# Kernel tuning notes

Measured on AMD Instinct MI355X. Metric: run time of the kernel, lower is better.

Reference implementation:

```python
import jax, jax.numpy as jnp
import numpy as np

G, N, DEG = 64, 2048, 8          # graphs, nodes/graph, avg degree
NTOT = G * N                      # 131072 nodes
E = NTOT * DEG                    # 1048576 edges
K = int(np.ceil(0.2 * N))         # 410 nodes kept per graph (SAGPooling ratio=0.2)
NK = G * K                        # 26240 pooled nodes
H, C = 3, 20                      # GAT heads, per-head channels
NEG_BIG = jnp.float32(-1e30)


def gcn(x, src, dst, W, b, n):
    """PyG GCNConv: x' = D^-1/2 (A+I) D^-1/2 x W + b (edge weight 1)."""
    h = x @ W
    deg = jax.ops.segment_sum(jnp.ones(src.shape[0], x.dtype), dst, num_segments=n) + 1.0
    dinv = jax.lax.rsqrt(deg)
    coef = dinv[src] * dinv[dst]                    # [E]
    agg = jax.ops.segment_sum(h[src] * coef[:, None], dst, num_segments=n)
    agg = agg + h * (dinv * dinv)[:, None]          # self loops
    return agg + b


def setup_inputs() -> dict:
    key = jax.random.key(0)
    ks = jax.random.split(key, 16)
    # edges constrained within each graph: per-graph local indices + offsets
    off = jnp.repeat(jnp.arange(G, dtype=jnp.int32) * N, N * DEG)   # [E]
    src = jax.random.randint(ks[0], (E,), 0, N, dtype=jnp.int32) + off
    dst = jax.random.randint(ks[1], (E,), 0, N, dtype=jnp.int32) + off
    batch = jnp.repeat(jnp.arange(G, dtype=jnp.int32), N)           # [NTOT]
    x = jax.random.normal(ks[2], (NTOT, 5), jnp.float32)
    s = 0.1
    return {
        "x": x, "src": src, "dst": dst, "batch": batch,
        "W1": jax.random.normal(ks[3], (5, 10)) * s,   "b1": jnp.zeros((10,)),
        "Ws": jax.random.normal(ks[4], (10, 1)) * s,   "bs": jnp.zeros((1,)),
        "Wg": jax.random.normal(ks[5], (10, H * C)) * s,
        "a_src": jax.random.normal(ks[6], (H, C)) * s,
        "a_dst": jax.random.normal(ks[7], (H, C)) * s,
        "bg": jnp.zeros((H * C,)),
        "Wf1": jax.random.normal(ks[8], (60, 30)) * s, "bf1": jnp.zeros((30,)),
        "Wf2": jax.random.normal(ks[9], (30, 3)) * s,  "bf2": jnp.zeros((3,)),
    }


def reference(x, src, dst, batch, W1, b1, Ws, bs, Wg, a_src, a_dst, bg, Wf1, bf1, Wf2, bf2):
    n = x.shape[0]
    # GCNConv(5,10)
    x1 = gcn(x, src, dst, W1, b1, n)                              # [NTOT,10]
    # SAGPooling: GCN scorer, top-k per graph, gate by tanh(score)
    score = gcn(x1, src, dst, Ws, bs, n)[:, 0]                    # [NTOT]
    _, topi = jax.lax.top_k(score.reshape(G, N), K)               # [G,K]
    perm = (topi + (jnp.arange(G) * N)[:, None]).reshape(-1)      # [NK] global ids
    xp = x1[perm] * jnp.tanh(score[perm])[:, None]                # [NK,10]
    # remap edges; drop (mask) edges touching removed nodes (filter_adj)
    new_idx = jnp.full((n,), -1, jnp.int32).at[perm].set(jnp.arange(NK, dtype=jnp.int32))
    s2, d2 = new_idx[src], new_idx[dst]
    emask = (s2 >= 0) & (d2 >= 0)
    s2 = jnp.where(emask, s2, 0)
    d2 = jnp.where(emask, d2, 0)
    # GATConv(10, 20, heads=3) with self loops
    h = (xp @ Wg).reshape(NK, H, C)
    al_s = jnp.sum(h * a_src, -1)                                 # [NK,H]
    al_d = jnp.sum(h * a_dst, -1)
    loop = jnp.arange(NK, dtype=jnp.int32)
    sa = jnp.concatenate([s2, loop])
    da = jnp.concatenate([d2, loop])
    ma = jnp.concatenate([emask, jnp.ones((NK,), bool)])
    logits = jax.nn.leaky_relu(al_s[sa] + al_d[da], 0.2)          # [E+NK,H]
    logits = jnp.where(ma[:, None], logits, NEG_BIG)
    mx = jax.ops.segment_max(logits, da, num_segments=NK)         # finite: self loops
    w = jnp.exp(logits - mx[da]) * ma[:, None]
    denom = jax.ops.segment_sum(w, da, num_segments=NK)
    alpha = w / denom[da]                                         # edge softmax
    out = jax.ops.segment_sum(h[sa] * alpha[..., None], da, num_segments=NK)  # [NK,H,C]
    xg = out.reshape(NK, H * C) + bg                              # concat heads -> 60
    # scatter_add readout over graphs
    g = jax.ops.segment_sum(xg, batch[perm], num_segments=G)      # [G,60]
    # MLP + LogSoftmax
    z = jax.nn.relu(g @ Wf1 + bf1) @ Wf2 + bf2                    # [G,3]
    return jax.nn.log_softmax(z, axis=1)
```

## Files before the change

kernel.cpp:

```cpp
#include <hip/hip_runtime.h>
#include <math.h>

#define G    64
#define NPG  2048
#define NTOT (G * NPG)
#define EPG  (NPG * 8)
#define NE   (NTOT * 8)
#define KSEL 410
#define NH   3
#define NC   20
#define HC   60
#define FCAP 24
#define KPAD 512
#define RP   12

#define OFF_H1P   0
#define OFF_CSR   98304
#define OFF_HIST  131072
#define OFF_RS    139264
#define OFF_SK    147456
#define OFF_NEWL  155648
#define OFF_PERML 159744
#define OFF_WSUM  160568
#define OFF_FLAGS 160632
#define OFF_BUFK  160656
#define OFF_BUFI  160912
#define ARENA_SZ  161040
#define OFF_XP    0
#define OFF_FADJ  16400
#define OFF_FCNT  36080
#define OFF_HF    37728
#define OFF_ALS   139264
#define OFF_ALD   144184
#define OFF_WRED  149104
#define OFF_GOUT  151024
#define OFF_HID   151264

__device__ inline float leaky(float x) { return x >= 0.f ? x : 0.2f * x; }

__device__ inline int wave_incl_scan(int v) {
    int lane = threadIdx.x & 63;
#pragma unroll
    for (int d = 1; d < 64; d <<= 1) {
        int t = __shfl_up(v, d, 64);
        if (lane >= d) v += t;
    }
    return v;
}

__global__ __launch_bounds__(1024) void k_all(
    const float* __restrict__ x, const int* __restrict__ src, const int* __restrict__ dst,
    const float* __restrict__ W1, const float* __restrict__ b1,
    const float* __restrict__ Ws, const float* __restrict__ bs,
    const float* __restrict__ Wg, const float* __restrict__ a_srcw,
    const float* __restrict__ a_dstw, const float* __restrict__ bg,
    const float* __restrict__ Wf1, const float* __restrict__ bf1,
    const float* __restrict__ Wf2, const float* __restrict__ bf2,
    float* __restrict__ x1g, float* __restrict__ out)
{
    __shared__ __align__(16) char arena[ARENA_SZ];
    float*          h1p   = (float*)(arena + OFF_H1P);
    unsigned short* csrL  = (unsigned short*)(arena + OFF_CSR);
    int*            hist  = (int*)(arena + OFF_HIST);
    int*            rsL   = (int*)(arena + OFF_RS);
    unsigned*       skL   = (unsigned*)(arena + OFF_SK);
    unsigned short* newLs = (unsigned short*)(arena + OFF_NEWL);
    unsigned short* permL = (unsigned short*)(arena + OFF_PERML);
    int*            wsumL = (int*)(arena + OFF_WSUM);
    int*            flags = (int*)(arena + OFF_FLAGS);
    unsigned*       bufK  = (unsigned*)(arena + OFF_BUFK);
    unsigned short* bufI  = (unsigned short*)(arena + OFF_BUFI);
    float*          xpL   = (float*)(arena + OFF_XP);
    unsigned short* fadjL = (unsigned short*)(arena + OFF_FADJ);
    int*            fcntL = (int*)(arena + OFF_FCNT);
    float*          hfL   = (float*)(arena + OFF_HF);
    float*          alsL  = (float*)(arena + OFF_ALS);
    float*          aldL  = (float*)(arena + OFF_ALD);
    float*          wred  = (float*)(arena + OFF_WRED);
    float*          goutL = (float*)(arena + OFF_GOUT);
    float*          hidL  = (float*)(arena + OFF_HID);
#define bselS  flags[0]
#define bneedS flags[1]
#define curS   flags[2]
#define totS   flags[3]
#define bcntS  flags[4]
#define cnt2S  flags[5]

    int g = blockIdx.x, tid = threadIdx.x, wid = tid >> 6;
    int nbase = g * NPG, ebase = g * EPG;

    for (int i = tid; i < NPG; i += 1024) hist[i] = 0;
    for (int i = tid; i < NPG; i += 1024) {
        float xi[5];
#pragma unroll
        for (int k = 0; k < 5; k++) xi[k] = x[(size_t)(nbase + i) * 5 + k];
        float v[10];
#pragma unroll
        for (int j = 0; j < 10; j++) {
            float s = 0.f;
#pragma unroll
            for (int k = 0; k < 5; k++) s += xi[k] * W1[k * 10 + j];
            v[j] = s;
        }
        float4* row = (float4*)(h1p + i * RP);
        row[0] = make_float4(v[0], v[1], v[2], v[3]);
        row[1] = make_float4(v[4], v[5], v[6], v[7]);
        row[2] = make_float4(v[8], v[9], 0.f, 0.f);
    }
    __syncthreads();
    for (int e = tid; e < EPG; e += 1024)
        atomicAdd(&hist[dst[ebase + e] - nbase], 1);
    __syncthreads();
    {
        int b2 = tid * 2;
        int v0 = hist[b2], v1 = hist[b2 + 1];
        int s = v0 + v1;
        int incl = wave_incl_scan(s);
        if ((tid & 63) == 63) wsumL[wid] = incl;
        __syncthreads();
        if (tid == 0) {
            int a = 0;
#pragma unroll
            for (int w = 0; w < 16; w++) { int t = wsumL[w]; wsumL[w] = a; a += t; }
        }
        __syncthreads();
        int base = wsumL[wid] + incl - s;
        rsL[b2] = base;
        rsL[b2 + 1] = base + v0;
        h1p[b2 * RP + 10] = rsqrtf((float)v0 + 1.0f);
        h1p[(b2 + 1) * RP + 10] = rsqrtf((float)v1 + 1.0f);
        hist[b2] = 0; hist[b2 + 1] = 0;
    }
    __syncthreads();
    for (int e = tid; e < EPG; e += 1024) {
        int ee = ebase + e;
        int sl = src[ee] - nbase;
        int dl = dst[ee] - nbase;
        int pos = rsL[dl] + atomicAdd(&hist[dl], 1);
        csrL[pos] = (unsigned short)sl;
    }
    __syncthreads();

    for (int i = tid; i < NPG; i += 1024) {
        const float4* rowi = (const float4*)(h1p + i * RP);
        float4 s0 = rowi[0], s1 = rowi[1], s2 = rowi[2];
        float di = s2.z;
        float a0 = 0.f, a1 = 0.f, a2 = 0.f, a3 = 0.f, a4 = 0.f;
        float a5 = 0.f, a6 = 0.f, a7 = 0.f, a8 = 0.f, a9 = 0.f;
        int p0 = rsL[i], p1 = (i == NPG - 1) ? EPG : rsL[i + 1];
        for (int e = p0; e < p1; e++) {
            int s = csrL[e];
            const float4* rw = (const float4*)(h1p + s * RP);
            float4 r0 = rw[0], r1 = rw[1], r2 = rw[2];
            float dv = r2.z;
            a0 += r0.x * dv; a1 += r0.y * dv; a2 += r0.z * dv; a3 += r0.w * dv;
            a4 += r1.x * dv; a5 += r1.y * dv; a6 += r1.z * dv; a7 += r1.w * dv;
            a8 += r2.x * dv; a9 += r2.y * dv;
        }
        float d2 = di * di;
        float v[10];
        v[0] = a0 * di + s0.x * d2 + b1[0];
        v[1] = a1 * di + s0.y * d2 + b1[1];
        v[2] = a2 * di + s0.z * d2 + b1[2];
        v[3] = a3 * di + s0.w * d2 + b1[3];
        v[4] = a4 * di + s1.x * d2 + b1[4];
        v[5] = a5 * di + s1.y * d2 + b1[5];
        v[6] = a6 * di + s1.z * d2 + b1[6];
        v[7] = a7 * di + s1.w * d2 + b1[7];
        v[8] = a8 * di + s2.x * d2 + b1[8];
        v[9] = a9 * di + s2.y * d2 + b1[9];
        float dot = 0.f;
#pragma unroll
        for (int j = 0; j < 10; j++) dot += v[j] * Ws[j];
        float4* xr = (float4*)(x1g + (size_t)(nbase + i) * RP);
        xr[0] = make_float4(v[0], v[1], v[2], v[3]);
        xr[1] = make_float4(v[4], v[5], v[6], v[7]);
        xr[2] = make_float4(v[8], v[9], 0.f, 0.f);
        h1p[i * RP + 11] = dot;
    }
    __syncthreads();

    float bsv = bs[0];
    for (int i = tid; i < NPG; i += 1024) {
        float2 own = *(const float2*)(h1p + i * RP + 10);
        int p0 = rsL[i], p1 = (i == NPG - 1) ? EPG : rsL[i + 1];
        float a = 0.f;
        for (int e = p0; e < p1; e++) {
            float2 dh = *(const float2*)(h1p + csrL[e] * RP + 10);
            a += dh.x * dh.y;
        }
        float sc = own.x * a + own.y * own.x * own.x + bsv;
        unsigned u = __float_as_uint(sc);
        skL[i] = (u & 0x80000000u) ? ~u : (u | 0x80000000u);
        newLs[i] = 0xFFFFu;
        hist[i] = 0;
    }
    if (tid == 0) curS = 0;
    __syncthreads();

    for (int i = tid; i < NPG; i += 1024)
        atomicAdd(&hist[skL[i] >> 21], 1);
    __syncthreads();
    int need = KSEL;
    {
        int b2 = tid * 2;
        int v0 = hist[b2], v1 = hist[b2 + 1];
        hist[b2] = 0; hist[b2 + 1] = 0;
        int s = v0 + v1;
        int incl = wave_incl_scan(s);
        if ((tid & 63) == 63) wsumL[wid] = incl;
        __syncthreads();
        if (tid == 0) {
            int a = 0;
#pragma unroll
            for (int w = 0; w < 16; w++) { int t = wsumL[w]; wsumL[w] = a; a += t; }
            totS = a;
            cnt2S = 0;
        }
        __syncthreads();
        int base = wsumL[wid] + incl - s;
        int tot = totS;
        { int Sb = tot - base;        int Sb1 = Sb - v0; if (Sb >= need && Sb1 < need) { bselS = b2;     bneedS = need - Sb1; bcntS = v0; } }
        { int Sb = tot - (base + v0); int Sb1 = Sb - v1; if (Sb >= need && Sb1 < need) { bselS = b2 + 1; bneedS = need - Sb1; bcntS = v1; } }
        __syncthreads();
    }
    int bsel0 = bselS;
    need = bneedS;
    int bcnt = bcntS;
    int greaterCnt = KSEL - need;
    for (int i = tid; i < NPG; i += 1024) {
        unsigned k = skL[i];
        int b = (int)(k >> 21);
        if (b > bsel0) {
            int p = atomicAdd(&curS, 1);
            permL[p] = (unsigned short)i;
            newLs[i] = (unsigned short)p;
        } else if (b == bsel0 && bcnt <= 64) {
            int pos = atomicAdd(&cnt2S, 1);
            bufK[pos] = k;
            bufI[pos] = (unsigned short)i;
        }
    }
    __syncthreads();
    if (bcnt <= 64) {
        if (wid == 0) {
            unsigned k  = (tid < bcnt) ? bufK[tid] : 0u;
            unsigned ix = (tid < bcnt) ? (unsigned)bufI[tid] : 0xFFFFu;
            int rank = 0;
#pragma unroll 8
            for (int j = 0; j < 64; j++) {
                unsigned kj = __shfl(k, j, 64);
                unsigned ij = __shfl(ix, j, 64);
                if (kj > k || (kj == k && ij < ix)) rank++;
            }
            if (tid < bcnt && rank < need) {
                int p = greaterCnt + rank;
                permL[p] = (unsigned short)ix;
                newLs[ix] = (unsigned short)p;
            }
        }
    } else {
        unsigned prefix = (unsigned)bsel0;
        for (int lv = 1; lv < 3; lv++) {
            for (int i = tid; i < NPG; i += 1024) {
                unsigned k = skL[i];
                bool match; unsigned bb;
                if (lv == 1) { match = ((k >> 21) == prefix); bb = (k >> 10) & 0x7FFu; }
                else         { match = ((k >> 10) == prefix); bb = k & 0x3FFu; }
                if (match) atomicAdd(&hist[bb], 1);
            }
            __syncthreads();
            int b2 = tid * 2;
            int v0 = hist[b2], v1 = hist[b2 + 1];
            hist[b2] = 0; hist[b2 + 1] = 0;
            int s = v0 + v1;
            int incl = wave_incl_scan(s);
            if ((tid & 63) == 63) wsumL[wid] = incl;
            __syncthreads();
            if (tid == 0) {
                int a = 0;
#pragma unroll
                for (int w = 0; w < 16; w++) { int t = wsumL[w]; wsumL[w] = a; a += t; }
                totS = a;
            }
            __syncthreads();
            int base = wsumL[wid] + incl - s;
            int tot = totS;
            { int Sb = tot - base;        int Sb1 = Sb - v0; if (Sb >= need && Sb1 < need) { bselS = b2;     bneedS = need - Sb1; } }
            { int Sb = tot - (base + v0); int Sb1 = Sb - v1; if (Sb >= need && Sb1 < need) { bselS = b2 + 1; bneedS = need - Sb1; } }
            __syncthreads();
            if (lv == 1) prefix = (prefix << 11) | (unsigned)bselS;
            else         prefix = (prefix << 10) | (unsigned)bselS;
            need = bneedS;
            __syncthreads();
        }
        unsigned T = prefix;
        greaterCnt = KSEL - need;
        for (int i = tid; i < NPG; i += 1024) {
            unsigned k = skL[i];
            if ((k >> 21) == (unsigned)bsel0 && k > T) {
                int p = atomicAdd(&curS, 1);
                permL[p] = (unsigned short)i;
                newLs[i] = (unsigned short)p;
            }
        }
        {
            int b2 = tid * 2;
            int lc = 0, loc2[2];
#pragma unroll
            for (int k = 0; k < 2; k++)
                if (skL[b2 + k] == T) loc2[lc++] = b2 + k;
            __syncthreads();
            int incl = wave_incl_scan(lc);
            if ((tid & 63) == 63) wsumL[wid] = incl;
            __syncthreads();
            if (tid == 0) {
                int a = 0;
#pragma unroll
                for (int w = 0; w < 16; w++) { int t = wsumL[w]; wsumL[w] = a; a += t; }
            }
            __syncthreads();
            int rank0 = wsumL[wid] + incl - lc;
            for (int j = 0; j < lc; j++) {
                int rank = rank0 + j;
                if (rank < need) {
                    int p = greaterCnt + rank;
                    permL[p] = (unsigned short)loc2[j];
                    newLs[loc2[j]] = (unsigned short)p;
                }
            }
        }
    }
    __syncthreads();

    for (int p = tid; p < KSEL; p += 1024) {
        int iL = permL[p];
        unsigned k = skL[iL];
        unsigned u = (k & 0x80000000u) ? (k & 0x7FFFFFFFu) : ~k;
        float tt = tanhf(__uint_as_float(u));
        const float4* xr = (const float4*)(x1g + (size_t)(nbase + iL) * RP);
        float4 q0 = xr[0], q1 = xr[1], q2 = xr[2];
        float* xp = xpL + p * 10;
        xp[0] = q0.x * tt; xp[1] = q0.y * tt; xp[2] = q0.z * tt; xp[3] = q0.w * tt;
        xp[4] = q1.x * tt; xp[5] = q1.y * tt; xp[6] = q1.z * tt; xp[7] = q1.w * tt;
        xp[8] = q2.x * tt; xp[9] = q2.y * tt;
        int p0 = rsL[iL], p1 = (iL == NPG - 1) ? EPG : rsL[iL + 1];
        int c = 0;
        for (int e = p0; e < p1; e++) {
            unsigned short s2 = newLs[csrL[e]];
            if (s2 != 0xFFFFu && c < FCAP) fadjL[p * FCAP + c++] = s2;
        }
        fcntL[p] = c;
    }
    __syncthreads();

    for (int t = tid; t < KSEL * NH; t += 1024) {
        int p = t / NH, hh = t - p * NH;
        float xi[10];
#pragma unroll
        for (int k = 0; k < 10; k++) xi[k] = xpL[p * 10 + k];
        float v[NC];
        float as_ = 0.f, ad_ = 0.f;
#pragma unroll
        for (int c = 0; c < NC; c++) {
            int j = hh * NC + c;
            float vv = 0.f;
#pragma unroll
            for (int k = 0; k < 10; k++) vv += xi[k] * Wg[k * HC + j];
            v[c] = vv;
            as_ += vv * a_srcw[j];
            ad_ += vv * a_dstw[j];
        }
        float4* hr = (float4*)(hfL + p * HC + hh * NC);
#pragma unroll
        for (int q = 0; q < 5; q++)
            hr[q] = make_float4(v[4 * q], v[4 * q + 1], v[4 * q + 2], v[4 * q + 3]);
        alsL[p * NH + hh] = as_;
        aldL[p * NH + hh] = ad_;
    }
    __syncthreads();

    {
        float res[NC];
#pragma unroll
        for (int rnd = 0; rnd < 2; rnd++) {
            int task = rnd == 0 ? tid : 1024 + tid;
            bool on = rnd == 0 || tid < KPAD;
            int hh = task >> 9, p = task & (KPAD - 1);
            if (on) {
                if (p < KSEL) {
                    float aldp = aldL[p * NH + hh];
                    float lself = leaky(alsL[p * NH + hh] + aldp);
                    float m = lself;
                    int c = fcntL[p];
                    const unsigned short* f = fadjL + p * FCAP;
                    for (int e = 0; e < c; e++)
                        m = fmaxf(m, leaky(alsL[f[e] * NH + hh] + aldp));
                    float wself = expf(lself - m), wsum = wself;
                    const float4* hp = (const float4*)(hfL + p * HC + hh * NC);
                    float4 r0 = hp[0], r1 = hp[1], r2 = hp[2], r3 = hp[3], r4 = hp[4];
                    r0.x *= wself; r0.y *= wself; r0.z *= wself; r0.w *= wself;
                    r1.x *= wself; r1.y *= wself; r1.z *= wself; r1.w *= wself;
                    r2.x *= wself; r2.y *= wself; r2.z *= wself; r2.w *= wself;
                    r3.x *= wself; r3.y *= wself; r3.z *= wself; r3.w *= wself;
                    r4.x *= wself; r4.y *= wself; r4.z *= wself; r4.w *= wself;
                    for (int e = 0; e < c; e++) {
                        int s2 = f[e];
                        float w = expf(leaky(alsL[s2 * NH + hh] + aldp) - m);
                        wsum += w;
                        const float4* hq = (const float4*)(hfL + s2 * HC + hh * NC);
                        float4 t0 = hq[0], t1 = hq[1], t2 = hq[2], t3 = hq[3], t4 = hq[4];
                        r0.x += w * t0.x; r0.y += w * t0.y; r0.z += w * t0.z; r0.w += w * t0.w;
                        r1.x += w * t1.x; r1.y += w * t1.y; r1.z += w * t1.z; r1.w += w * t1.w;
                        r2.x += w * t2.x; r2.y += w * t2.y; r2.z += w * t2.z; r2.w += w * t2.w;
                        r3.x += w * t3.x; r3.y += w * t3.y; r3.z += w * t3.z; r3.w += w * t3.w;
                        r4.x += w * t4.x; r4.y += w * t4.y; r4.z += w * t4.z; r4.w += w * t4.w;
                    }
                    float inv = 1.f / wsum;
                    res[0] = r0.x * inv;  res[1] = r0.y * inv;  res[2] = r0.z * inv;  res[3] = r0.w * inv;
                    res[4] = r1.x * inv;  res[5] = r1.y * inv;  res[6] = r1.z * inv;  res[7] = r1.w * inv;
                    res[8] = r2.x * inv;  res[9] = r2.y * inv;  res[10] = r2.z * inv; res[11] = r2.w * inv;
                    res[12] = r3.x * inv; res[13] = r3.y * inv; res[14] = r3.z * inv; res[15] = r3.w * inv;
                    res[16] = r4.x * inv; res[17] = r4.y * inv; res[18] = r4.z * inv; res[19] = r4.w * inv;
                } else {
#pragma unroll
                    for (int cc = 0; cc < NC; cc++) res[cc] = 0.f;
                }
#pragma unroll
                for (int cc = 0; cc < NC; cc++) {
                    float v = res[cc];
#pragma unroll
                    for (int d = 1; d < 64; d <<= 1) v += __shfl_xor(v, d, 64);
                    res[cc] = v;
                }
                if ((tid & 63) == 0) {
                    int slot = rnd == 0 ? hh * 8 + (wid & 7) : 16 + wid;
#pragma unroll
                    for (int cc = 0; cc < NC; cc++) wred[slot * NC + cc] = res[cc];
                }
            }
        }
    }
    __syncthreads();
    if (tid < HC) {
        int hh = tid / NC, c = tid - hh * NC;
        float a = 0.f;
#pragma unroll
        for (int w = 0; w < 8; w++) a += wred[(hh * 8 + w) * NC + c];
        goutL[tid] = a + (float)KSEL * bg[tid];
    }
    __syncthreads();

    if (tid < 30) {
        float s = bf1[tid];
#pragma unroll
        for (int k = 0; k < HC; k++) s += goutL[k] * Wf1[k * 30 + tid];
        hidL[tid] = s > 0.f ? s : 0.f;
    }
    __syncthreads();
    if (tid == 0) {
        float z[3];
#pragma unroll
        for (int j = 0; j < 3; j++) {
            float s = bf2[j];
            for (int k = 0; k < 30; k++) s += hidL[k] * Wf2[k * 3 + j];
            z[j] = s;
        }
        float m = fmaxf(z[0], fmaxf(z[1], z[2]));
        float lse = logf(expf(z[0] - m) + expf(z[1] - m) + expf(z[2] - m)) + m;
#pragma unroll
        for (int j = 0; j < 3; j++) out[g * 3 + j] = z[j] - lse;
    }
}

extern "C" void kernel_launch(void* const* d_in, const int* in_sizes, int n_in,
                              void* d_out, int out_size, void* d_ws, size_t ws_size,
                              hipStream_t stream) {
    const float* x     = (const float*)d_in[0];
    const int*   src   = (const int*)d_in[1];
    const int*   dst   = (const int*)d_in[2];
    const float* W1    = (const float*)d_in[4];
    const float* b1    = (const float*)d_in[5];
    const float* Ws    = (const float*)d_in[6];
    const float* bs    = (const float*)d_in[7];
    const float* Wg    = (const float*)d_in[8];
    const float* a_src = (const float*)d_in[9];
    const float* a_dst = (const float*)d_in[10];
    const float* bg    = (const float*)d_in[11];
    const float* Wf1   = (const float*)d_in[12];
    const float* bf1   = (const float*)d_in[13];
    const float* Wf2   = (const float*)d_in[14];
    const float* bf2   = (const float*)d_in[15];
    float* out = (float*)d_out;

    float* x1g = (float*)d_ws;

    k_all<<<G, 1024, 0, stream>>>(x, src, dst, W1, b1, Ws, bs, Wg, a_src, a_dst,
                                  bg, Wf1, bf1, Wf2, bf2, x1g, out);
}
```

Measured before the change: 145.4 us.

## Split fused per-graph kernel into front, score and tail kernels across more blocks

Replaces the single per-graph 64-block kernel with three kernels. The first GCN layer and CSR build now run on four blocks per graph, each handling a quarter of the destination nodes. A separate score kernel computes the SAGPool scores, and a tail kernel does top-k, GAT and readout per graph. The aim is to occupy more compute units than the 64 blocks of the fused kernel could. The cost is that each front block redundantly recomputes the full-graph h1 and histogram, CSR and intermediates now round-trip through global memory, and two extra launches are added. The per-chunk CSR buffer is capped at a fixed size and drops edges silently if a chunk overflows it.

Result: slower. 151.9 us (+4.5%).

```diff
diff --git a/kernel.cpp b/kernel.cpp
--- a/kernel.cpp
+++ b/kernel.cpp
@@ -13,28 +13,9 @@
 #define FCAP 24
 #define KPAD 512
 #define RP   12
-
-#define OFF_H1P   0
-#define OFF_CSR   98304
-#define OFF_HIST  131072
-#define OFF_RS    139264
-#define OFF_SK    147456
-#define OFF_NEWL  155648
-#define OFF_PERML 159744
-#define OFF_WSUM  160568
-#define OFF_FLAGS 160632
-#define OFF_BUFK  160656
-#define OFF_BUFI  160912
-#define ARENA_SZ  161040
-#define OFF_XP    0
-#define OFF_FADJ  16400
-#define OFF_FCNT  36080
-#define OFF_HF    37728
-#define OFF_ALS   139264
-#define OFF_ALD   144184
-#define OFF_WRED  149104
-#define OFF_GOUT  151024
-#define OFF_HID   151264
+#define CPG  4
+#define NCK  (NPG / CPG)
+#define CSCAP 5632
 
 __device__ inline float leaky(float x) { return x >= 0.f ? x : 0.2f * x; }
 
@@ -48,46 +29,21 @@
     return v;
 }
 
-__global__ __launch_bounds__(1024) void k_all(
+__global__ __launch_bounds__(1024) void k_front(
     const float* __restrict__ x, const int* __restrict__ src, const int* __restrict__ dst,
-    const float* __restrict__ W1, const float* __restrict__ b1,
-    const float* __restrict__ Ws, const float* __restrict__ bs,
-    const float* __restrict__ Wg, const float* __restrict__ a_srcw,
-    const float* __restrict__ a_dstw, const float* __restrict__ bg,
-    const float* __restrict__ Wf1, const float* __restrict__ bf1,
-    const float* __restrict__ Wf2, const float* __restrict__ bf2,
-    float* __restrict__ x1g, float* __restrict__ out)
+    const float* __restrict__ W1, const float* __restrict__ b1, const float* __restrict__ Ws,
+    float* __restrict__ x1g, float* __restrict__ hsg, float* __restrict__ dinvg,
+    int* __restrict__ rowptrg, unsigned short* __restrict__ csrg)
 {
-    __shared__ __align__(16) char arena[ARENA_SZ];
-    float*          h1p   = (float*)(arena + OFF_H1P);
-    unsigned short* csrL  = (unsigned short*)(arena + OFF_CSR);
-    int*            hist  = (int*)(arena + OFF_HIST);
-    int*            rsL   = (int*)(arena + OFF_RS);
-    unsigned*       skL   = (unsigned*)(arena + OFF_SK);
-    unsigned short* newLs = (unsigned short*)(arena + OFF_NEWL);
-    unsigned short* permL = (unsigned short*)(arena + OFF_PERML);
-    int*            wsumL = (int*)(arena + OFF_WSUM);
-    int*            flags = (int*)(arena + OFF_FLAGS);
-    unsigned*       bufK  = (unsigned*)(arena + OFF_BUFK);
-    unsigned short* bufI  = (unsigned short*)(arena + OFF_BUFI);
-    float*          xpL   = (float*)(arena + OFF_XP);
-    unsigned short* fadjL = (unsigned short*)(arena + OFF_FADJ);
-    int*            fcntL = (int*)(arena + OFF_FCNT);
-    float*          hfL   = (float*)(arena + OFF_HF);
-    float*          alsL  = (float*)(arena + OFF_ALS);
-    float*          aldL  = (float*)(arena + OFF_ALD);
-    float*          wred  = (float*)(arena + OFF_WRED);
-    float*          goutL = (float*)(arena + OFF_GOUT);
-    float*          hidL  = (float*)(arena + OFF_HID);
-#define bselS  flags[0]
-#define bneedS flags[1]
-#define curS   flags[2]
-#define totS   flags[3]
-#define bcntS  flags[4]
-#define cnt2S  flags[5]
-
-    int g = blockIdx.x, tid = threadIdx.x, wid = tid >> 6;
+    __shared__ __align__(16) float h1p[NPG * RP];
+    __shared__ int hist[NPG];
+    __shared__ int rs[NPG];
+    __shared__ unsigned short csrC[CSCAP];
+    __shared__ int wsumL[16];
+    int tid = threadIdx.x, wid = tid >> 6;
+    int g = blockIdx.x >> 2, ck = blockIdx.x & 3;
     int nbase = g * NPG, ebase = g * EPG;
+    int nlo = ck * NCK, nhi = nlo + NCK;
 
     for (int i = tid; i < NPG; i += 1024) hist[i] = 0;
     for (int i = tid; i < NPG; i += 1024) {
@@ -125,31 +81,46 @@
         }
         __syncthreads();
         int base = wsumL[wid] + incl - s;
-        rsL[b2] = base;
-        rsL[b2 + 1] = base + v0;
+        rs[b2] = base;
+        rs[b2 + 1] = base + v0;
         h1p[b2 * RP + 10] = rsqrtf((float)v0 + 1.0f);
         h1p[(b2 + 1) * RP + 10] = rsqrtf((float)v1 + 1.0f);
         hist[b2] = 0; hist[b2 + 1] = 0;
     }
     __syncthreads();
+    int csbase = rs[nlo];
+    int csend = (nhi == NPG) ? EPG : rs[nhi];
+    if (tid < NCK) {
+        int i = nlo + tid;
+        rowptrg[nbase + i] = ebase + rs[i];
+        dinvg[nbase + i] = h1p[i * RP + 10];
+    }
+    if (blockIdx.x == G * CPG - 1 && tid == 0) rowptrg[NTOT] = NE;
     for (int e = tid; e < EPG; e += 1024) {
         int ee = ebase + e;
-        int sl = src[ee] - nbase;
         int dl = dst[ee] - nbase;
-        int pos = rsL[dl] + atomicAdd(&hist[dl], 1);
-        csrL[pos] = (unsigned short)sl;
-    }
-    __syncthreads();
-
-    for (int i = tid; i < NPG; i += 1024) {
+        if (dl >= nlo && dl < nhi) {
+            int sl = src[ee] - nbase;
+            int pos = rs[dl] - csbase + atomicAdd(&hist[dl], 1);
+            if (pos < CSCAP) csrC[pos] = (unsigned short)sl;
+        }
+    }
+    __syncthreads();
+    {
+        int cnt = csend - csbase;
+        for (int w = tid; w < cnt; w += 1024) csrg[ebase + csbase + w] = csrC[w];
+    }
+    if (tid < NCK) {
+        int i = nlo + tid;
         const float4* rowi = (const float4*)(h1p + i * RP);
         float4 s0 = rowi[0], s1 = rowi[1], s2 = rowi[2];
         float di = s2.z;
         float a0 = 0.f, a1 = 0.f, a2 = 0.f, a3 = 0.f, a4 = 0.f;
         float a5 = 0.f, a6 = 0.f, a7 = 0.f, a8 = 0.f, a9 = 0.f;
-        int p0 = rsL[i], p1 = (i == NPG - 1) ? EPG : rsL[i + 1];
+        int p0 = rs[i] - csbase;
+        int p1 = ((i == nhi - 1) ? csend : rs[i + 1]) - csbase;
         for (int e = p0; e < p1; e++) {
-            int s = csrL[e];
+            int s = csrC[e];
             const float4* rw = (const float4*)(h1p + s * RP);
             float4 r0 = rw[0], r1 = rw[1], r2 = rw[2];
             float dv = r2.z;
@@ -176,36 +147,106 @@
         xr[0] = make_float4(v[0], v[1], v[2], v[3]);
         xr[1] = make_float4(v[4], v[5], v[6], v[7]);
         xr[2] = make_float4(v[8], v[9], 0.f, 0.f);
-        h1p[i * RP + 11] = dot;
-    }
-    __syncthreads();
-
-    float bsv = bs[0];
+        hsg[nbase + i] = dot;
+    }
+}
+
+__global__ __launch_bounds__(512) void k_score(
+    const float* __restrict__ hsg, const float* __restrict__ dinvg,
+    const int* __restrict__ rowptrg, const unsigned short* __restrict__ csrg,
+    const float* __restrict__ bs, float* __restrict__ scoreg)
+{
+    __shared__ float2 dh[NPG];
+    int tid = threadIdx.x;
+    int g = blockIdx.x >> 2, ck = blockIdx.x & 3;
+    int nbase = g * NPG;
+    for (int i = tid; i < NPG; i += 512)
+        dh[i] = make_float2(dinvg[nbase + i], hsg[nbase + i]);
+    __syncthreads();
+    int i = ck * NCK + tid;
+    float di = dh[i].x;
+    int p0 = rowptrg[nbase + i], p1 = rowptrg[nbase + i + 1];
+    float a = 0.f;
+    for (int e = p0; e < p1; e++) {
+        float2 t = dh[csrg[e]];
+        a += t.x * t.y;
+    }
+    scoreg[nbase + i] = di * a + dh[i].y * di * di + bs[0];
+}
+
+#define TOFF_FADJ  0
+#define TOFF_FCNT  19680
+#define TOFF_XP    21328
+#define TOFF_WRED  21328
+#define TOFF_GOUT  23248
+#define TOFF_HID   23488
+#define TOFF_HF    37728
+#define TOFF_BINS  37728
+#define TOFF_ALS   136128
+#define TOFF_ALD   141048
+#define TOFF_SK    145968
+#define TOFF_NEWL  154160
+#define TOFF_PERML 158256
+#define TOFF_WSUM  159080
+#define TOFF_FLAGS 159144
+#define TOFF_BUFK  159168
+#define TOFF_BUFI  159424
+#define TARENA_SZ  159552
+
+__global__ __launch_bounds__(1024) void k_tail(
+    const float* __restrict__ scoreg, const float* __restrict__ x1g,
+    const int* __restrict__ rowptrg, const unsigned short* __restrict__ csrg,
+    const float* __restrict__ Wg, const float* __restrict__ a_srcw,
+    const float* __restrict__ a_dstw, const float* __restrict__ bg,
+    const float* __restrict__ Wf1, const float* __restrict__ bf1,
+    const float* __restrict__ Wf2, const float* __restrict__ bf2,
+    float* __restrict__ out)
+{
+    __shared__ __align__(16) char arena[TARENA_SZ];
+    unsigned short* fadjL = (unsigned short*)(arena + TOFF_FADJ);
+    int*            fcntL = (int*)(arena + TOFF_FCNT);
+    float*          xpL   = (float*)(arena + TOFF_XP);
+    float*          wred  = (float*)(arena + TOFF_WRED);
+    float*          goutL = (float*)(arena + TOFF_GOUT);
+    float*          hidL  = (float*)(arena + TOFF_HID);
+    float*          hfL   = (float*)(arena + TOFF_HF);
+    int*            bins  = (int*)(arena + TOFF_BINS);
+    float*          alsL  = (float*)(arena + TOFF_ALS);
+    float*          aldL  = (float*)(arena + TOFF_ALD);
+    unsigned*       skL   = (unsigned*)(arena + TOFF_SK);
+    unsigned short* newLs = (unsigned short*)(arena + TOFF_NEWL);
+    unsigned short* permL = (unsigned short*)(arena + TOFF_PERML);
+    int*            wsumL = (int*)(arena + TOFF_WSUM);
+    int*            flags = (int*)(arena + TOFF_FLAGS);
+    unsigned*       bufK  = (unsigned*)(arena + TOFF_BUFK);
+    unsigned short* bufI  = (unsigned short*)(arena + TOFF_BUFI);
+#define bselS  flags[0]
+#define bneedS flags[1]
+#define curS   flags[2]
+#define totS   flags[3]
+#define bcntS  flags[4]
+#define cnt2S  flags[5]
+
+    int g = blockIdx.x, tid = threadIdx.x, wid = tid >> 6;
+    int nbase = g * NPG;
+
     for (int i = tid; i < NPG; i += 1024) {
-        float2 own = *(const float2*)(h1p + i * RP + 10);
-        int p0 = rsL[i], p1 = (i == NPG - 1) ? EPG : rsL[i + 1];
-        float a = 0.f;
-        for (int e = p0; e < p1; e++) {
-            float2 dh = *(const float2*)(h1p + csrL[e] * RP + 10);
-            a += dh.x * dh.y;
-        }
-        float sc = own.x * a + own.y * own.x * own.x + bsv;
-        unsigned u = __float_as_uint(sc);
+        unsigned u = __float_as_uint(scoreg[nbase + i]);
         skL[i] = (u & 0x80000000u) ? ~u : (u | 0x80000000u);
         newLs[i] = 0xFFFFu;
-        hist[i] = 0;
+        bins[i] = 0;
     }
     if (tid == 0) curS = 0;
     __syncthreads();
 
     for (int i = tid; i < NPG; i += 1024)
-        atomicAdd(&hist[skL[i] >> 21], 1);
+        atomicAdd(&bins[skL[i] >> 21], 1);
     __syncthreads();
     int need = KSEL;
     {
         int b2 = tid * 2;
-        int v0 = hist[b2], v1 = hist[b2 + 1];
-        hist[b2] = 0; hist[b2 + 1] = 0;
+        int v0 = bins[b2], v1 = bins[b2 + 1];
+        bins[b2] = 0; bins[b2 + 1] = 0;
         int s = v0 + v1;
         int incl = wave_incl_scan(s);
         if ((tid & 63) == 63) wsumL[wid] = incl;
@@ -267,12 +308,12 @@
                 bool match; unsigned bb;
                 if (lv == 1) { match = ((k >> 21) == prefix); bb = (k >> 10) & 0x7FFu; }
                 else         { match = ((k >> 10) == prefix); bb = k & 0x3FFu; }
-                if (match) atomicAdd(&hist[bb], 1);
+                if (match) atomicAdd(&bins[bb], 1);
             }
             __syncthreads();
             int b2 = tid * 2;
-            int v0 = hist[b2], v1 = hist[b2 + 1];
-            hist[b2] = 0; hist[b2 + 1] = 0;
+            int v0 = bins[b2], v1 = bins[b2 + 1];
+            bins[b2] = 0; bins[b2 + 1] = 0;
             int s = v0 + v1;
             int incl = wave_incl_scan(s);
             if ((tid & 63) == 63) wsumL[wid] = incl;
@@ -344,10 +385,10 @@
         xp[0] = q0.x * tt; xp[1] = q0.y * tt; xp[2] = q0.z * tt; xp[3] = q0.w * tt;
         xp[4] = q1.x * tt; xp[5] = q1.y * tt; xp[6] = q1.z * tt; xp[7] = q1.w * tt;
         xp[8] = q2.x * tt; xp[9] = q2.y * tt;
-        int p0 = rsL[iL], p1 = (iL == NPG - 1) ? EPG : rsL[iL + 1];
+        int p0 = rowptrg[nbase + iL], p1 = rowptrg[nbase + iL + 1];
         int c = 0;
         for (int e = p0; e < p1; e++) {
-            unsigned short s2 = newLs[csrL[e]];
+            unsigned short s2 = newLs[csrg[e]];
             if (s2 != 0xFFFFu && c < FCAP) fadjL[p * FCAP + c++] = s2;
         }
         fcntL[p] = c;
@@ -493,8 +534,18 @@
     const float* bf2   = (const float*)d_in[15];
     float* out = (float*)d_out;
 
-    float* x1g = (float*)d_ws;
-
-    k_all<<<G, 1024, 0, stream>>>(x, src, dst, W1, b1, Ws, bs, Wg, a_src, a_dst,
-                                  bg, Wf1, bf1, Wf2, bf2, x1g, out);
+    const size_t N = NTOT;
+    float* ws = (float*)d_ws;
+    float* x1g    = ws;
+    float* hsg    = x1g + (size_t)RP * N;
+    float* dinvg  = hsg + N;
+    float* scoreg = dinvg + N;
+    int* rowptrg  = (int*)(scoreg + N);
+    unsigned short* csrg = (unsigned short*)(rowptrg + N + 2);
+
+    k_front<<<G * CPG, 1024, 0, stream>>>(x, src, dst, W1, b1, Ws,
+                                          x1g, hsg, dinvg, rowptrg, csrg);
+    k_score<<<G * CPG, 512, 0, stream>>>(hsg, dinvg, rowptrg, csrg, bs, scoreg);
+    k_tail<<<G, 1024, 0, stream>>>(scoreg, x1g, rowptrg, csrg, Wg, a_src, a_dst,
+                                   bg, Wf1, bf1, Wf2, bf2, out);
 }
```
